# Optimization experiments

Measured on AMD Instinct MI355X. Metric: run time of the kernel, lower is better.

The kernel has to match this reference:

```python
import jax, jax.numpy as jnp
import numpy as np

B, L, H, S, D = 2, 4096, 16, 64, 128  # batch, seq, num_heads, num_states, head_dim


def setup_inputs() -> dict:
    key = jax.random.key(0)
    k1, k2, k3 = jax.random.split(key, 3)
    return {
        "x": jax.random.normal(k1, (B, L, H, D), dtype=jnp.float32),
        "weight": jax.random.normal(k2, (H, S, D), dtype=jnp.float32),   # nn.Parameter torch.randn
        "bias": jax.random.normal(k3, (H, S), dtype=jnp.float32),
    }


def reference(x, weight, bias):
    b, l, h, d = x.shape
    s = weight.shape[1]
    T = b * l
    # per-head linear router in fp32 (matches x.float()/weight.float() in torch)
    logits = jnp.einsum('blhd,hsd->blhs', x.astype(jnp.float32), weight.astype(jnp.float32)) \
             + bias.astype(jnp.float32)
    score = jax.nn.softmax(logits, axis=-1)                # [B,L,H,S]
    indices = jnp.argmax(score, axis=-1).astype(jnp.int32)  # [B,L,H]
    # GradTop1 forward: all-ones; straight-through backward scatters grad at argmax.
    top = jnp.take_along_axis(score, indices[..., None], axis=-1)[..., 0]
    sg_indices = top - jax.lax.stop_gradient(top) + 1.0      # forward == 1, grad -> one-hot scatter
    # histogram per head over num_states (Triton bincount equivalent)
    flat = indices.reshape(T, h)                             # [T,H]
    counts = jax.vmap(lambda v: jnp.bincount(v, length=s))(flat.T)  # [H,S]
    mean_indices = counts.astype(jnp.float32) / T
    balance_loss = s * jnp.sum(jnp.mean(mean_indices[None, None] * score, axis=(0, 1)))
    return sg_indices.astype(x.dtype), indices, balance_loss.astype(x.dtype)
```

## Files before the change

kernel.cpp:

```cpp
#include <hip/hip_runtime.h>


#define TOKENS  8192
#define NHEAD   16
#define NSTATE  64
#define DDIM    128
#define TH      (TOKENS * NHEAD)

#define WFRAG_BYTES (1u << 19)
#define BFRAG_OFF   WFRAG_BYTES
#define BFRAG_BYTES 4096
#define REP_OFF     (WFRAG_BYTES + BFRAG_BYTES)
#define REP_BYTES   65536
#define IDX_OFF     (REP_OFF + REP_BYTES)

typedef _Float16 half8  __attribute__((ext_vector_type(8)));
typedef float    f32x4  __attribute__((ext_vector_type(4)));
typedef float    f32x16 __attribute__((ext_vector_type(16)));

#define GLOAD_LDS16(gsrc, ldst)                                           \
    __builtin_amdgcn_global_load_lds(                                     \
        (const __attribute__((address_space(1))) void*)(gsrc),            \
        (__attribute__((address_space(3))) void*)(ldst), 16, 0, 0)

__device__ __forceinline__ void split8(const f32x4 v0, const f32x4 v1,
                                       half8& hh, half8& ll) {
    #pragma unroll
    for (int j = 0; j < 4; ++j) {
        _Float16 h0 = (_Float16)v0[j];
        hh[j]     = h0;  ll[j]     = (_Float16)(v0[j] - (float)h0);
        _Float16 h1 = (_Float16)v1[j];
        hh[4 + j] = h1;  ll[4 + j] = (_Float16)(v1[j] - (float)h1);
    }
}

__device__ __forceinline__ float dpp_sum32(float v) {
    float t;
    t = __int_as_float(__builtin_amdgcn_update_dpp(0, __float_as_int(v), 0x111, 0xf, 0xf, true)); v += t;
    t = __int_as_float(__builtin_amdgcn_update_dpp(0, __float_as_int(v), 0x112, 0xf, 0xf, true)); v += t;
    t = __int_as_float(__builtin_amdgcn_update_dpp(0, __float_as_int(v), 0x114, 0xf, 0xf, true)); v += t;
    t = __int_as_float(__builtin_amdgcn_update_dpp(0, __float_as_int(v), 0x118, 0xf, 0xf, true)); v += t;
    t = __int_as_float(__builtin_amdgcn_update_dpp(0, __float_as_int(v), 0x142, 0xf, 0xf, true)); v += t;
    return v;
}

__global__ __launch_bounds__(256)
void prep_w(const float* __restrict__ w, const float* __restrict__ bias,
            half8* __restrict__ wfrag, float* __restrict__ bfrag,
            float* __restrict__ rep)
{
    const int t = blockIdx.x * 256 + threadIdx.x;
    rep[t] = 0.0f;
    const int lane  = t & 63;
    const int half_ = (t >> 6) & 1;
    const int ks    = (t >> 7) & 7;
    const int h     = t >> 10;
    const int s     = half_ * 32 + (lane & 31);
    const int k0    = ks * 16 + (lane >> 5) * 8;
    const float* src = w + (size_t)(h * NSTATE + s) * DDIM + k0;
    f32x4 v0 = *reinterpret_cast<const f32x4*>(src);
    f32x4 v1 = *reinterpret_cast<const f32x4*>(src + 4);
    half8 hv, lv;
    split8(v0, v1, hv, lv);
    const size_t fb = (size_t)h * 2048 + (size_t)((ks * 4 + half_ * 2)) * 64;
    wfrag[fb + lane]      = hv;
    wfrag[fb + 64 + lane] = lv;

    if (t < 1024) {
        const int h2 = t >> 6, hi2 = (t >> 5) & 1, j = t & 31;
        const int tau = j >> 4, r = j & 15;
        const int s2 = (r & 3) + ((r >> 2) << 3) + (hi2 << 2) + (tau << 5);
        bfrag[t] = bias[h2 * NSTATE + s2];
    }
}

__global__ __launch_bounds__(256)
void router_mfma(const float* __restrict__ x,
                 const half8* __restrict__ wfrag,
                 const float* __restrict__ bfrag,
                 float* __restrict__ idx_scr,
                 float* __restrict__ repf,
                 float* __restrict__ repc)
{
    __shared__ __align__(16) unsigned char smem[32768];
    __shared__ unsigned int hist[64];
    __shared__ __align__(16) float ssums[4][64];

    const int blk  = blockIdx.x;
    const int h    = blk & 15;
    const int grp  = blk >> 4;
    const int tid  = threadIdx.x;
    const int wave = __builtin_amdgcn_readfirstlane(tid >> 6);
    const int lane = tid & 63;
    const int tk   = lane & 31;
    const int hi   = lane >> 5;
    const int tokb = grp * 128 + wave * 32;

    {
        const char* wsrc = (const char*)wfrag + (size_t)h * 32768;
        #pragma unroll
        for (int i = 0; i < 8; ++i) {
            const int off = (i * 256 + tid) * 16;
            GLOAD_LDS16(wsrc + off, smem + off);
        }
    }
    if (tid < 64) hist[tid] = 0;

    const float* bf = bfrag + ((h << 1) | hi) * 32;
    f32x16 acc0, acc1;
    #pragma unroll
    for (int r = 0; r < 16; ++r) { acc0[r] = bf[r]; acc1[r] = bf[16 + r]; }

    const float* xrow = x + (size_t)(tokb + tk) * (NHEAD * DDIM) + h * DDIM + hi * 8;

    __syncthreads();

    #pragma unroll
    for (int ks = 0; ks < 8; ++ks) {
        half8 wh0 = *reinterpret_cast<const half8*>(smem + (ks * 4 + 0) * 1024 + lane * 16);
        half8 wl0 = *reinterpret_cast<const half8*>(smem + (ks * 4 + 1) * 1024 + lane * 16);
        half8 wh1 = *reinterpret_cast<const half8*>(smem + (ks * 4 + 2) * 1024 + lane * 16);
        half8 wl1 = *reinterpret_cast<const half8*>(smem + (ks * 4 + 3) * 1024 + lane * 16);
        f32x4 g0 = *reinterpret_cast<const f32x4*>(xrow + ks * 16);
        f32x4 g1 = *reinterpret_cast<const f32x4*>(xrow + ks * 16 + 4);
        half8 xh, xl;
        split8(g0, g1, xh, xl);
        acc0 = __builtin_amdgcn_mfma_f32_32x32x16_f16(wh0, xh, acc0, 0, 0, 0);
        acc0 = __builtin_amdgcn_mfma_f32_32x32x16_f16(wh0, xl, acc0, 0, 0, 0);
        acc0 = __builtin_amdgcn_mfma_f32_32x32x16_f16(wl0, xh, acc0, 0, 0, 0);
        acc1 = __builtin_amdgcn_mfma_f32_32x32x16_f16(wh1, xh, acc1, 0, 0, 0);
        acc1 = __builtin_amdgcn_mfma_f32_32x32x16_f16(wh1, xl, acc1, 0, 0, 0);
        acc1 = __builtin_amdgcn_mfma_f32_32x32x16_f16(wl1, xh, acc1, 0, 0, 0);
    }

    float mx = acc1[15];
    #pragma unroll
    for (int r = 14; r >= 0; --r) mx = fmaxf(mx, acc1[r]);
    #pragma unroll
    for (int r = 15; r >= 0; --r) mx = fmaxf(mx, acc0[r]);

    int idx = 0;
    #pragma unroll
    for (int r = 15; r >= 0; --r) {
        const int s = 32 + (r & 3) + ((r >> 2) << 3) + (hi << 2);
        idx = (acc1[r] == mx) ? s : idx;
    }
    #pragma unroll
    for (int r = 15; r >= 0; --r) {
        const int s = (r & 3) + ((r >> 2) << 3) + (hi << 2);
        idx = (acc0[r] == mx) ? s : idx;
    }
    {
        const float omx  = __shfl_xor(mx, 32);
        const int   oidx = __shfl_xor(idx, 32);
        if (omx > mx || (omx == mx && oidx < idx)) { mx = omx; idx = oidx; }
    }

    float sm = 0.f;
    #pragma unroll
    for (int r = 0; r < 16; ++r) { acc0[r] = __expf(acc0[r]); sm += acc0[r]; }
    #pragma unroll
    for (int r = 0; r < 16; ++r) { acc1[r] = __expf(acc1[r]); sm += acc1[r]; }
    sm += __shfl_xor(sm, 32);
    const float rinv = __builtin_amdgcn_rcpf(sm);

    #pragma unroll
    for (int r = 0; r < 16; ++r) {
        acc0[r] = dpp_sum32(acc0[r] * rinv);
        acc1[r] = dpp_sum32(acc1[r] * rinv);
    }
    if ((lane & 31) == 31) {
        #pragma unroll
        for (int g = 0; g < 4; ++g) {
            f32x4 p0, p1;
            #pragma unroll
            for (int i = 0; i < 4; ++i) { p0[i] = acc0[g * 4 + i]; p1[i] = acc1[g * 4 + i]; }
            *reinterpret_cast<f32x4*>(&ssums[wave][(g << 3) + (hi << 2)])      = p0;
            *reinterpret_cast<f32x4*>(&ssums[wave][32 + (g << 3) + (hi << 2)]) = p1;
        }
    }

    if (hi == 0) {
        atomicAdd(&hist[idx], 1u);
        idx_scr[(size_t)h * TOKENS + tokb + tk] = (float)idx;
    }

    __syncthreads();
    if (wave == 0) {
        const float sv = ssums[0][lane] + ssums[1][lane] + ssums[2][lane] + ssums[3][lane];
        const float cv = (float)hist[lane];
        const int rep = blk & 7;
        atomicAdd(repf + rep * 1024 + h * 64 + lane, sv);
        atomicAdd(repc + rep * 1024 + h * 64 + lane, cv);
    }
}

__global__ __launch_bounds__(256)
void finale(const float* __restrict__ idx_scr,
            const float* __restrict__ repf,
            const float* __restrict__ repc,
            float* __restrict__ out)
{
    const int b   = blockIdx.x;
    const int tid = threadIdx.x;

    if (b < 32) {
        __shared__ float tl[256 * 17];
        #pragma unroll
        for (int hh = 0; hh < 16; ++hh)
            tl[tid * 17 + hh] = idx_scr[(size_t)hh * TOKENS + b * 256 + tid];
        __syncthreads();
        #pragma unroll
        for (int k = 0; k < 16; ++k) {
            const int i = k * 256 + tid;
            out[(size_t)TH + (size_t)b * 4096 + i] = tl[(i >> 4) * 17 + (i & 15)];
            out[(size_t)b * 4096 + i] = 1.0f;
        }
    } else {
        float part = 0.0f;
        for (int j = tid; j < NHEAD * NSTATE; j += 256) {
            float cf = 0.f, cc = 0.f;
            #pragma unroll
            for (int r = 0; r < 8; ++r) {
                cf += repf[r * 1024 + j];
                cc += repc[r * 1024 + j];
            }
            part += cf * cc;
        }
        #pragma unroll
        for (int d = 1; d <= 32; d <<= 1)
            part += __shfl_xor(part, d);
        __shared__ float red[4];
        const int wv = tid >> 6, lane = tid & 63;
        if (lane == 0) red[wv] = part;
        __syncthreads();
        if (tid == 0) {
            const float tot = red[0] + red[1] + red[2] + red[3];
            const float T = (float)TOKENS;
            out[2 * (size_t)TH] = tot * ((float)NSTATE / (T * T));
        }
    }
}

extern "C" void kernel_launch(void* const* d_in, const int* in_sizes, int n_in,
                              void* d_out, int out_size, void* d_ws, size_t ws_size,
                              hipStream_t stream)
{
    const float* x    = (const float*)d_in[0];
    const float* w    = (const float*)d_in[1];
    const float* bias = (const float*)d_in[2];
    float* out = (float*)d_out;

    half8* wfrag   = (half8*)d_ws;
    float* bfrag   = (float*)((char*)d_ws + BFRAG_OFF);
    float* rep     = (float*)((char*)d_ws + REP_OFF);
    float* repf    = rep;
    float* repc    = rep + 8192;
    float* idx_scr = (float*)((char*)d_ws + IDX_OFF);

    prep_w<<<dim3(64), dim3(256), 0, stream>>>(w, bias, wfrag, bfrag, rep);
    router_mfma<<<dim3(1024), dim3(256), 0, stream>>>(x, wfrag, bfrag,
                                                      idx_scr, repf, repc);
    finale<<<dim3(33), dim3(256), 0, stream>>>(idx_scr, repf, repc, out);
}
```

Baseline: 29.39 us.

## Fuse weight prep into router kernel, use exp2 with pre-scaled weights, widen finale grid

Drops the separate prep_w kernel. Each router block now loads its head's fp32 weights and bias directly, scales them by log2(e), splits them into fp16 hi/lo pairs and writes them into LDS, so the softmax can use exp2f. The accumulator zeroing moves to a hipMemsetAsync, and the finale transpose is spread over 256 small blocks instead of 32 large ones. This removes a kernel launch and the workspace round trip, but every one of the 1024 blocks now repeats the conversion work and the global weight reads.

New measurement: 32.44 us. 1.1x slower.

```diff
diff --git a/kernel.cpp b/kernel.cpp
--- a/kernel.cpp
+++ b/kernel.cpp
@@ -7,21 +7,14 @@
 #define DDIM    128
 #define TH      (TOKENS * NHEAD)
 
-#define WFRAG_BYTES (1u << 19)
-#define BFRAG_OFF   WFRAG_BYTES
-#define BFRAG_BYTES 4096
-#define REP_OFF     (WFRAG_BYTES + BFRAG_BYTES)
-#define REP_BYTES   65536
-#define IDX_OFF     (REP_OFF + REP_BYTES)
+#define REP_BYTES 65536
+#define IDX_OFF   REP_BYTES
+
+#define LOG2E 1.4426950408889634f
 
 typedef _Float16 half8  __attribute__((ext_vector_type(8)));
 typedef float    f32x4  __attribute__((ext_vector_type(4)));
 typedef float    f32x16 __attribute__((ext_vector_type(16)));
-
-#define GLOAD_LDS16(gsrc, ldst)                                           \
-    __builtin_amdgcn_global_load_lds(                                     \
-        (const __attribute__((address_space(1))) void*)(gsrc),            \
-        (__attribute__((address_space(3))) void*)(ldst), 16, 0, 0)
 
 __device__ __forceinline__ void split8(const f32x4 v0, const f32x4 v1,
                                        half8& hh, half8& ll) {
@@ -45,44 +38,15 @@
 }
 
 __global__ __launch_bounds__(256)
-void prep_w(const float* __restrict__ w, const float* __restrict__ bias,
-            half8* __restrict__ wfrag, float* __restrict__ bfrag,
-            float* __restrict__ rep)
-{
-    const int t = blockIdx.x * 256 + threadIdx.x;
-    rep[t] = 0.0f;
-    const int lane  = t & 63;
-    const int half_ = (t >> 6) & 1;
-    const int ks    = (t >> 7) & 7;
-    const int h     = t >> 10;
-    const int s     = half_ * 32 + (lane & 31);
-    const int k0    = ks * 16 + (lane >> 5) * 8;
-    const float* src = w + (size_t)(h * NSTATE + s) * DDIM + k0;
-    f32x4 v0 = *reinterpret_cast<const f32x4*>(src);
-    f32x4 v1 = *reinterpret_cast<const f32x4*>(src + 4);
-    half8 hv, lv;
-    split8(v0, v1, hv, lv);
-    const size_t fb = (size_t)h * 2048 + (size_t)((ks * 4 + half_ * 2)) * 64;
-    wfrag[fb + lane]      = hv;
-    wfrag[fb + 64 + lane] = lv;
-
-    if (t < 1024) {
-        const int h2 = t >> 6, hi2 = (t >> 5) & 1, j = t & 31;
-        const int tau = j >> 4, r = j & 15;
-        const int s2 = (r & 3) + ((r >> 2) << 3) + (hi2 << 2) + (tau << 5);
-        bfrag[t] = bias[h2 * NSTATE + s2];
-    }
-}
-
-__global__ __launch_bounds__(256)
-void router_mfma(const float* __restrict__ x,
-                 const half8* __restrict__ wfrag,
-                 const float* __restrict__ bfrag,
-                 float* __restrict__ idx_scr,
-                 float* __restrict__ repf,
-                 float* __restrict__ repc)
+void router_all(const float* __restrict__ x,
+                const float* __restrict__ w,
+                const float* __restrict__ bias,
+                float* __restrict__ idx_scr,
+                float* __restrict__ repf,
+                float* __restrict__ repc)
 {
     __shared__ __align__(16) unsigned char smem[32768];
+    __shared__ float        lds_bias[64];
     __shared__ unsigned int hist[64];
     __shared__ __align__(16) float ssums[4][64];
 
@@ -96,24 +60,38 @@
     const int hi   = lane >> 5;
     const int tokb = grp * 128 + wave * 32;
 
-    {
-        const char* wsrc = (const char*)wfrag + (size_t)h * 32768;
-        #pragma unroll
-        for (int i = 0; i < 8; ++i) {
-            const int off = (i * 256 + tid) * 16;
-            GLOAD_LDS16(wsrc + off, smem + off);
-        }
-    }
-    if (tid < 64) hist[tid] = 0;
-
-    const float* bf = bfrag + ((h << 1) | hi) * 32;
+    #pragma unroll
+    for (int j = 0; j < 4; ++j) {
+        const int fp    = wave * 4 + j;
+        const int ks    = fp >> 1, half_ = fp & 1;
+        const int s     = half_ * 32 + tk;
+        const int k0    = ks * 16 + hi * 8;
+        const float* src = w + (size_t)(h * NSTATE + s) * DDIM + k0;
+        f32x4 v0 = *reinterpret_cast<const f32x4*>(src);
+        f32x4 v1 = *reinterpret_cast<const f32x4*>(src + 4);
+        #pragma unroll
+        for (int i = 0; i < 4; ++i) { v0[i] *= LOG2E; v1[i] *= LOG2E; }
+        half8 hv, lv;
+        split8(v0, v1, hv, lv);
+        *reinterpret_cast<half8*>(smem + (fp * 2)     * 1024 + lane * 16) = hv;
+        *reinterpret_cast<half8*>(smem + (fp * 2 + 1) * 1024 + lane * 16) = lv;
+    }
+    if (tid < 64) {
+        lds_bias[tid] = bias[h * NSTATE + tid] * LOG2E;
+        hist[tid] = 0;
+    }
+    __syncthreads();
+
     f32x16 acc0, acc1;
     #pragma unroll
-    for (int r = 0; r < 16; ++r) { acc0[r] = bf[r]; acc1[r] = bf[16 + r]; }
+    for (int g = 0; g < 4; ++g) {
+        f32x4 b0 = *reinterpret_cast<const f32x4*>(&lds_bias[g * 8 + hi * 4]);
+        f32x4 b1 = *reinterpret_cast<const f32x4*>(&lds_bias[32 + g * 8 + hi * 4]);
+        #pragma unroll
+        for (int i = 0; i < 4; ++i) { acc0[g * 4 + i] = b0[i]; acc1[g * 4 + i] = b1[i]; }
+    }
 
     const float* xrow = x + (size_t)(tokb + tk) * (NHEAD * DDIM) + h * DDIM + hi * 8;
-
-    __syncthreads();
 
     #pragma unroll
     for (int ks = 0; ks < 8; ++ks) {
@@ -158,9 +136,9 @@
 
     float sm = 0.f;
     #pragma unroll
-    for (int r = 0; r < 16; ++r) { acc0[r] = __expf(acc0[r]); sm += acc0[r]; }
-    #pragma unroll
-    for (int r = 0; r < 16; ++r) { acc1[r] = __expf(acc1[r]); sm += acc1[r]; }
+    for (int r = 0; r < 16; ++r) { acc0[r] = exp2f(acc0[r]); sm += acc0[r]; }
+    #pragma unroll
+    for (int r = 0; r < 16; ++r) { acc1[r] = exp2f(acc1[r]); sm += acc1[r]; }
     sm += __shfl_xor(sm, 32);
     const float rinv = __builtin_amdgcn_rcpf(sm);
 
@@ -204,17 +182,18 @@
     const int b   = blockIdx.x;
     const int tid = threadIdx.x;
 
-    if (b < 32) {
-        __shared__ float tl[256 * 17];
-        #pragma unroll
-        for (int hh = 0; hh < 16; ++hh)
-            tl[tid * 17 + hh] = idx_scr[(size_t)hh * TOKENS + b * 256 + tid];
+    if (b < 256) {
+        __shared__ float tl[32][17];
+        const int tk = tid & 31, hh = tid >> 5;
+        #pragma unroll
+        for (int i = 0; i < 2; ++i)
+            tl[tk][i * 8 + hh] = idx_scr[(size_t)(i * 8 + hh) * TOKENS + b * 32 + tk];
         __syncthreads();
         #pragma unroll
-        for (int k = 0; k < 16; ++k) {
-            const int i = k * 256 + tid;
-            out[(size_t)TH + (size_t)b * 4096 + i] = tl[(i >> 4) * 17 + (i & 15)];
-            out[(size_t)b * 4096 + i] = 1.0f;
+        for (int i = 0; i < 2; ++i) {
+            const int o = i * 256 + tid;
+            out[(size_t)TH + (size_t)b * 512 + o] = tl[o >> 4][o & 15];
+            out[(size_t)b * 512 + o] = 1.0f;
         }
     } else {
         float part = 0.0f;
@@ -251,15 +230,12 @@
     const float* bias = (const float*)d_in[2];
     float* out = (float*)d_out;
 
-    half8* wfrag   = (half8*)d_ws;
-    float* bfrag   = (float*)((char*)d_ws + BFRAG_OFF);
-    float* rep     = (float*)((char*)d_ws + REP_OFF);
-    float* repf    = rep;
-    float* repc    = rep + 8192;
+    float* repf    = (float*)d_ws;
+    float* repc    = (float*)d_ws + 8192;
     float* idx_scr = (float*)((char*)d_ws + IDX_OFF);
 
-    prep_w<<<dim3(64), dim3(256), 0, stream>>>(w, bias, wfrag, bfrag, rep);
-    router_mfma<<<dim3(1024), dim3(256), 0, stream>>>(x, wfrag, bfrag,
-                                                      idx_scr, repf, repc);
-    finale<<<dim3(33), dim3(256), 0, stream>>>(idx_scr, repf, repc, out);
-}
+    hipMemsetAsync(d_ws, 0, REP_BYTES, stream);
+    router_all<<<dim3(1024), dim3(256), 0, stream>>>(x, w, bias,
+                                                     idx_scr, repf, repc);
+    finale<<<dim3(257), dim3(256), 0, stream>>>(idx_scr, repf, repc, out);
+}
```
